# Kernel optimization log

Measured on AMD Instinct MI355X. Metric: run time of the kernel, lower is better.

The kernel has to match this reference:

```python
import jax, jax.numpy as jnp
import numpy as np

HQ, HK, D = 16, 4, 64
WINDOW = 1024  # sliding-window left size; right=0 (causal)
GATE_CH = 12
RMS_EPS = 1e-8


def rms_norm(x):
    return x * jax.lax.rsqrt(jnp.mean(x * x, axis=-1, keepdims=True) + RMS_EPS)


def apply_rope(x, cos, sin):
    # x: [B,T,H,D]; cos/sin: [T,D//2] broadcast to [1,T,1,D//2]
    x1, x2 = jnp.split(x, 2, axis=-1)
    c = cos[None, :, None, :]
    s = sin[None, :, None, :]
    return jnp.concatenate([x1 * c - x2 * s, x1 * s + x2 * c], axis=-1)


def setup_inputs() -> dict:
    key = jax.random.key(0)
    ks = jax.random.split(key, 7)
    B, T, E = 2, 2048, HQ * D
    x = jax.random.normal(ks[0], (B, T, E), jnp.float32)
    value_embeds = jax.random.normal(ks[1], (B, T, HK * D), jnp.float32)
    # rope cache: angles for half the head dim
    inv_freq = 1.0 / (10000.0 ** (jnp.arange(D // 2, dtype=jnp.float32) / (D // 2)))
    ang = jnp.arange(T, dtype=jnp.float32)[:, None] * inv_freq[None, :]
    rope_cos = jnp.cos(ang)
    rope_sin = jnp.sin(ang)
    std = (3.0 ** 0.5) * (E ** -0.5)
    w_qkv = jax.random.uniform(ks[2], ((HQ + 2 * HK) * D, E), jnp.float32, -std, std)
    w_gate = jax.random.normal(ks[3], (HK, GATE_CH), jnp.float32) * 0.02
    w_o = jax.random.normal(ks[4], (E, E), jnp.float32) * 0.02
    return {"x": x, "value_embeds": value_embeds, "rope_cos": rope_cos,
            "rope_sin": rope_sin, "w_qkv": w_qkv, "w_gate": w_gate, "w_o": w_o}


def reference(x, value_embeds, rope_cos, rope_sin, w_qkv, w_gate, w_o):
    B, T, E = x.shape
    groups = HQ // HK
    qkv = jnp.einsum('bte,fe->btf', x, w_qkv).reshape(B, T, HQ + 2 * HK, D)
    q = qkv[:, :, :HQ, :]
    k = qkv[:, :, HQ:HQ + HK, :]
    v = qkv[:, :, HQ + HK:, :]
    # value-embedding gating
    ve = value_embeds.reshape(B, T, HK, D)
    gate = 3.0 * jax.nn.sigmoid(jnp.einsum('btc,hc->bth', x[..., :GATE_CH], w_gate))
    v = v + gate[..., None] * ve
    # rope + qk-norm
    q = rms_norm(apply_rope(q, rope_cos, rope_sin))
    k = rms_norm(apply_rope(k, rope_cos, rope_sin))
    # GQA: repeat kv heads
    k_rep = jnp.repeat(k, groups, axis=2)  # [B,T,HQ,D]
    v_rep = jnp.repeat(v, groups, axis=2)
    scale = 1.0 / jnp.sqrt(jnp.float32(D))
    scores = jnp.einsum('bqhd,bkhd->bhqk', q, k_rep) * scale
    i = jnp.arange(T)[:, None]
    j = jnp.arange(T)[None, :]
    mask = (j <= i) & (j >= i - WINDOW)  # causal + sliding window
    scores = jnp.where(mask[None, None], scores, jnp.float32(-1e30))
    attn = jax.nn.softmax(scores, axis=-1)
    out = jnp.einsum('bhqk,bkhd->bqhd', attn, v_rep).reshape(B, T, E)
    out = jnp.einsum('bte,fe->btf', out, w_o)
    return out
```

## Files before the change

kernel.cpp:

```cpp
#include <hip/hip_runtime.h>
#include <math.h>

#define T_LEN 2048
#define NB 2
#define E_DIM 1024
#define F_DIM 1536
#define HQn 16
#define HKn 4
#define Dh 64
#define WIN 1024
#define GATE_CH 12
#define PS 72

typedef unsigned short u16;
typedef unsigned int u32;
typedef __attribute__((ext_vector_type(8))) short bf16x8;
typedef __attribute__((ext_vector_type(4))) short bf16x4;
typedef __attribute__((ext_vector_type(4))) float f32x4;

#if __has_builtin(__builtin_amdgcn_mfma_f32_16x16x16bf16_1k)
#define MFMA16(A, B, C) __builtin_amdgcn_mfma_f32_16x16x16bf16_1k(A, B, C, 0, 0, 0)
#elif __has_builtin(__builtin_amdgcn_mfma_f32_16x16x16_bf16)
#define MFMA16(A, B, C) __builtin_amdgcn_mfma_f32_16x16x16_bf16(A, B, C, 0, 0, 0)
#else
static __device__ __forceinline__ f32x4 mfma16_asm(bf16x4 a, bf16x4 b, f32x4 c) {
  f32x4 d;
  asm volatile("s_nop 1\n\tv_mfma_f32_16x16x16_bf16 %0, %1, %2, %3\n\ts_nop 7\n\ts_nop 7"
               : "=v"(d) : "v"(a), "v"(b), "v"(c));
  return d;
}
#define MFMA16(A, B, C) mfma16_asm(A, B, C)
#endif

__device__ __forceinline__ u16 f2bf(float f) {
  union { float f; unsigned int u; } v; v.f = f;
  unsigned int u = v.u + 0x7FFF + ((v.u >> 16) & 1);
  return (u16)(u >> 16);
}
__device__ __forceinline__ float bf2f(u16 h) {
  union { unsigned int u; float f; } v; v.u = ((unsigned int)h) << 16;
  return v.f;
}
__device__ __forceinline__ u32 pack_bf2(float hi, float lo) {
  union { float f; u32 u; } a, b; a.f = hi; b.f = lo;
  return __builtin_amdgcn_perm(a.u + 0x8000u, b.u + 0x8000u, 0x07060302u);
}
__device__ __forceinline__ void async_copy16(const void* g, void* l) {
  __builtin_amdgcn_global_load_lds(
      (const __attribute__((address_space(1))) unsigned int*)g,
      (__attribute__((address_space(3))) unsigned int*)l, 16, 0, 0);
}

__global__ __launch_bounds__(256) void cvt_all(
    const float4* __restrict__ x, const float4* __restrict__ wqkv,
    const float4* __restrict__ wo, uint2* __restrict__ xb,
    uint2* __restrict__ wqb, uint2* __restrict__ wob)
{
  int blk = blockIdx.x;
  const float4* in; uint2* out; int i;
  if (blk < 4096)       { in = x;    out = xb;  i = blk * 256 + threadIdx.x; }
  else if (blk < 5632)  { in = wqkv; out = wqb; i = (blk - 4096) * 256 + threadIdx.x; }
  else                  { in = wo;   out = wob; i = (blk - 5632) * 256 + threadIdx.x; }
  float4 v = in[i];
  uint2 o;
  o.x = (unsigned)f2bf(v.x) | ((unsigned)f2bf(v.y) << 16);
  o.y = (unsigned)f2bf(v.z) | ((unsigned)f2bf(v.w) << 16);
  out[i] = o;
}

template<int BM, int BN, int STORE_BF16>
__global__ __launch_bounds__(256) void gemm_bf16(
    const u16* __restrict__ A, const u16* __restrict__ B,
    void* __restrict__ Cv, int M, int N, int K)
{
  constexpr int MI = BM / 32, NJ = BN / 32;
  __shared__ u16 As[BM * 32];
  __shared__ u16 Bs[BN * 32];
  const int tid = threadIdx.x;
  const int wave = tid >> 6, lane = tid & 63;
  const int quad = lane >> 4, lanelow = lane & 15;
  const int row0 = blockIdx.x * BM;
  const int col0 = blockIdx.y * BN;
  const int wm = (wave >> 1) * (BM / 2), wn = (wave & 1) * (BN / 2);

  f32x4 acc[MI][NJ];
#pragma unroll
  for (int i = 0; i < MI; ++i)
#pragma unroll
    for (int j = 0; j < NJ; ++j) acc[i][j] = (f32x4){0.f, 0.f, 0.f, 0.f};

  const int r1 = wave * 16 + (lane >> 2);
  const int c1 = (lane & 3) * 8;

  for (int k0 = 0; k0 < K; k0 += 32) {
    __syncthreads();
#pragma unroll
    for (int p = 0; p < BM / 64; ++p)
      async_copy16(A + (size_t)(row0 + r1 + p * 64) * K + k0 + c1,
                   &As[(r1 + p * 64) * 32 + c1]);
#pragma unroll
    for (int p = 0; p < BN / 64; ++p)
      async_copy16(B + (size_t)(col0 + r1 + p * 64) * K + k0 + c1,
                   &Bs[(r1 + p * 64) * 32 + c1]);
    __syncthreads();

    bf16x8 a[MI], b[NJ];
#pragma unroll
    for (int i = 0; i < MI; ++i)
      a[i] = *(const bf16x8*)&As[(wm + i * 16 + lanelow) * 32 + quad * 8];
#pragma unroll
    for (int j = 0; j < NJ; ++j)
      b[j] = *(const bf16x8*)&Bs[(wn + j * 16 + lanelow) * 32 + quad * 8];
#pragma unroll
    for (int i = 0; i < MI; ++i)
#pragma unroll
      for (int j = 0; j < NJ; ++j)
        acc[i][j] = __builtin_amdgcn_mfma_f32_16x16x32_bf16(a[i], b[j], acc[i][j], 0, 0, 0);
  }

#pragma unroll
  for (int i = 0; i < MI; ++i)
#pragma unroll
    for (int j = 0; j < NJ; ++j) {
      int r = row0 + wm + i * 16 + quad * 4;
      int c = col0 + wn + j * 16 + lanelow;
#pragma unroll
      for (int reg = 0; reg < 4; ++reg) {
        if (STORE_BF16)
          ((u16*)Cv)[(size_t)(r + reg) * N + c] = f2bf(acc[i][j][reg]);
        else
          ((float*)Cv)[(size_t)(r + reg) * N + c] = acc[i][j][reg];
      }
    }
}

__global__ __launch_bounds__(256) void postproc_bf(
    const u16* __restrict__ qkv, const float* __restrict__ x,
    const float* __restrict__ ve, const float* __restrict__ rcos,
    const float* __restrict__ rsin, const float* __restrict__ wg,
    u16* __restrict__ qa, u16* __restrict__ ka, u16* __restrict__ va)
{
  const int token = blockIdx.x;
  const int t = token & (T_LEN - 1);
  const int tid = threadIdx.x;
  const int wave = tid >> 6, lane = tid & 63;
  __shared__ float gate[HKn];
  if (tid < HKn) {
    float g = 0.f;
#pragma unroll
    for (int c = 0; c < GATE_CH; ++c)
      g += x[(size_t)token * E_DIM + c] * wg[tid * GATE_CH + c];
    gate[tid] = 3.f / (1.f + __expf(-g));
  }
  __syncthreads();
  const int half = lane & 31;
  for (int vi = wave; vi < HQn + HKn; vi += 4) {
    const u16* p = qkv + (size_t)token * F_DIM + vi * Dh;
    float c = rcos[t * 32 + half], s = rsin[t * 32 + half];
    float x1 = bf2f(p[half]), x2 = bf2f(p[half + 32]);
    float y = (lane < 32) ? (x1 * c - x2 * s) : (x1 * s + x2 * c);
    float ss = y * y;
#pragma unroll
    for (int o = 32; o; o >>= 1) ss += __shfl_xor(ss, o, 64);
    float v = y * rsqrtf(ss * (1.f / Dh) + 1e-8f);
    if (vi < HQn)
      qa[((size_t)token * HQn + vi) * Dh + lane] = f2bf(v * 0.1803368801f);
    else
      ka[((size_t)token * HKn + (vi - HQn)) * Dh + lane] = f2bf(v);
  }
  {
    float g = gate[tid >> 6];
    size_t vidx = (size_t)token * (HKn * Dh) + tid;
    va[vidx] = f2bf(bf2f(qkv[(size_t)token * F_DIM + (HQn + HKn) * Dh + tid]) + g * ve[vidx]);
  }
}

__global__ __launch_bounds__(256) void transpose_v(
    const u16* __restrict__ va, u16* __restrict__ vt)
{
  __shared__ u16 tile[64][PS];
  const int bhk = blockIdx.y;
  const int b = bhk >> 2, hk = bhk & 3;
  const int t0 = blockIdx.x * 64;
  const int tid = threadIdx.x;
#pragma unroll
  for (int p = 0; p < 2; ++p) {
    int s = tid + p * 256;
    int r = s >> 3, seg = s & 7;
    *(uint4*)&tile[r][seg * 8] =
        *(const uint4*)(va + ((size_t)(b * T_LEN + t0 + r) * HKn + hk) * Dh + seg * 8);
  }
  __syncthreads();
#pragma unroll
  for (int p = 0; p < 2; ++p) {
    int s = tid + p * 256;
    int d = s >> 3, seg = s & 7;
    u16 tmp[8];
#pragma unroll
    for (int e = 0; e < 8; ++e) tmp[e] = tile[seg * 8 + e][d];
    *(uint4*)(vt + ((size_t)bhk * Dh + d) * T_LEN + t0 + seg * 8) = *(uint4*)tmp;
  }
}

__global__ __launch_bounds__(256) void attn_mfma(
    const u16* __restrict__ qa, const u16* __restrict__ ka,
    const u16* __restrict__ vt_g, u16* __restrict__ att)
{
  __shared__ u16 Ks[2][64 * PS];
  __shared__ u16 Vt[2][64 * PS];
  const int qt = blockIdx.x, h = blockIdx.y, b = blockIdx.z;
  const int hk = h >> 2;
  const int qb = qt * 64;
  const int tid = threadIdx.x;
  const int wave = tid >> 6, lane = tid & 63;
  const int quad = lane >> 4, lanelow = lane & 15;

  bf16x8 aQ[2];
#pragma unroll
  for (int kk = 0; kk < 2; ++kk)
    aQ[kk] = *(const bf16x8*)(qa +
        ((size_t)(b * T_LEN + qb + wave * 16 + lanelow) * HQn + h) * Dh +
        kk * 32 + quad * 8);

  f32x4 O[4];
  float l = 0.f;
#pragma unroll
  for (int dt = 0; dt < 4; ++dt) O[dt] = (f32x4){0.f, 0.f, 0.f, 0.f};

  const int kt0 = (qt >= 16) ? qt - 16 : 0;
  const int kt1 = qt;

  const int sr0 = tid >> 3,         sc0 = (tid & 7) * 8;
  const int sr1 = (tid + 256) >> 3, sc1 = ((tid + 256) & 7) * 8;
  const u16* kg = ka + (size_t)(b * T_LEN) * (HKn * Dh) + hk * Dh;
  const u16* vg = vt_g + (size_t)(b * HKn + hk) * Dh * T_LEN;

  {
    const int kb = kt0 * 64;
    uint4 k0 = *(const uint4*)(kg + (size_t)(kb + sr0) * (HKn * Dh) + sc0);
    uint4 k1 = *(const uint4*)(kg + (size_t)(kb + sr1) * (HKn * Dh) + sc1);
    uint4 v0 = *(const uint4*)(vg + (size_t)sr0 * T_LEN + kb + sc0);
    uint4 v1 = *(const uint4*)(vg + (size_t)sr1 * T_LEN + kb + sc1);
    *(uint4*)&Ks[0][sr0 * PS + sc0] = k0;
    *(uint4*)&Ks[0][sr1 * PS + sc1] = k1;
    *(uint4*)&Vt[0][sr0 * PS + sc0] = v0;
    *(uint4*)&Vt[0][sr1 * PS + sc1] = v1;
  }

  for (int kt = kt0; kt <= kt1; ++kt) {
    const int buf = (kt - kt0) & 1;
    const int kb = kt * 64;
    uint4 k0, k1, v0, v1;
    const bool more = (kt < kt1);
    if (more) {
      const int nb = kb + 64;
      k0 = *(const uint4*)(kg + (size_t)(nb + sr0) * (HKn * Dh) + sc0);
      k1 = *(const uint4*)(kg + (size_t)(nb + sr1) * (HKn * Dh) + sc1);
      v0 = *(const uint4*)(vg + (size_t)sr0 * T_LEN + nb + sc0);
      v1 = *(const uint4*)(vg + (size_t)sr1 * T_LEN + nb + sc1);
    }
    __syncthreads();

    f32x4 St[4];
#pragma unroll
    for (int jt = 0; jt < 4; ++jt) {
      bf16x8 aK0 = *(const bf16x8*)&Ks[buf][(jt * 16 + lanelow) * PS + quad * 8];
      bf16x8 aK1 = *(const bf16x8*)&Ks[buf][(jt * 16 + lanelow) * PS + 32 + quad * 8];
      f32x4 acc = (f32x4){-12.f, -12.f, -12.f, -12.f};
      acc = __builtin_amdgcn_mfma_f32_16x16x32_bf16(aK0, aQ[0], acc, 0, 0, 0);
      acc = __builtin_amdgcn_mfma_f32_16x16x32_bf16(aK1, aQ[1], acc, 0, 0, 0);
      St[jt] = acc;
    }
    if (kt == kt1) {
#pragma unroll
      for (int jt = 0; jt < 4; ++jt)
#pragma unroll
        for (int rr = 0; rr < 4; ++rr) {
          int ig = qb + wave * 16 + lanelow;
          int jg = kb + jt * 16 + quad * 4 + rr;
          if (jg > ig) St[jt][rr] = -1e30f;
        }
    } else if (kt == kt0 && qt >= 16) {
#pragma unroll
      for (int jt = 0; jt < 4; ++jt)
#pragma unroll
        for (int rr = 0; rr < 4; ++rr) {
          int ig = qb + wave * 16 + lanelow;
          int jg = kb + jt * 16 + quad * 4 + rr;
          if (jg < ig - WIN) St[jt][rr] = -1e30f;
        }
    }
    bf16x4 Pt[4];
#pragma unroll
    for (int jt = 0; jt < 4; ++jt) {
      float p0 = __builtin_amdgcn_exp2f(St[jt][0]);
      float p1 = __builtin_amdgcn_exp2f(St[jt][1]);
      float p2 = __builtin_amdgcn_exp2f(St[jt][2]);
      float p3 = __builtin_amdgcn_exp2f(St[jt][3]);
      l += (p0 + p1) + (p2 + p3);
      union { uint2 u; bf16x4 v; } pu;
      pu.u.x = pack_bf2(p1, p0);
      pu.u.y = pack_bf2(p3, p2);
      Pt[jt] = pu.v;
    }
#pragma unroll
    for (int dt = 0; dt < 4; ++dt)
#pragma unroll
      for (int jt = 0; jt < 4; ++jt) {
        bf16x4 aV = *(const bf16x4*)&Vt[buf][(dt * 16 + lanelow) * PS + jt * 16 + quad * 4];
        O[dt] = MFMA16(aV, Pt[jt], O[dt]);
      }
    if (more) {
      const int nbuf = buf ^ 1;
      *(uint4*)&Ks[nbuf][sr0 * PS + sc0] = k0;
      *(uint4*)&Ks[nbuf][sr1 * PS + sc1] = k1;
      *(uint4*)&Vt[nbuf][sr0 * PS + sc0] = v0;
      *(uint4*)&Vt[nbuf][sr1 * PS + sc1] = v1;
    }
  }

  {
    float s = l;
    s += __shfl_xor(s, 16, 64);
    s += __shfl_xor(s, 32, 64);
    float inv = 1.f / s;
    int qg = qb + wave * 16 + lanelow;
    u16* obase = att + (size_t)(b * T_LEN + qg) * E_DIM + h * Dh;
#pragma unroll
    for (int dt = 0; dt < 4; ++dt) {
      bf16x4 ov;
      ov[0] = (short)f2bf(O[dt][0] * inv);
      ov[1] = (short)f2bf(O[dt][1] * inv);
      ov[2] = (short)f2bf(O[dt][2] * inv);
      ov[3] = (short)f2bf(O[dt][3] * inv);
      *(bf16x4*)(obase + dt * 16 + quad * 4) = ov;
    }
  }
}

extern "C" void kernel_launch(void* const* d_in, const int* in_sizes, int n_in,
                              void* d_out, int out_size, void* d_ws, size_t ws_size,
                              hipStream_t stream)
{
  const float* x    = (const float*)d_in[0];
  const float* ve   = (const float*)d_in[1];
  const float* rc   = (const float*)d_in[2];
  const float* rs   = (const float*)d_in[3];
  const float* wqkv = (const float*)d_in[4];
  const float* wg   = (const float*)d_in[5];
  const float* wo   = (const float*)d_in[6];
  float* out = (float*)d_out;

  char* ws = (char*)d_ws;
  u16* x_bf    = (u16*)(ws);
  u16* v_t     = x_bf;
  u16* wqkv_bf = (u16*)(ws + 8388608);
  u16* wo_bf   = (u16*)(ws + 11534336);
  u16* qkv_bf  = (u16*)(ws + 13631488);
  u16* att     = qkv_bf;
  u16* q_att   = (u16*)(ws + 26214400);
  u16* k_att   = (u16*)(ws + 34603008);
  u16* v_att   = (u16*)(ws + 36700160);

  cvt_all<<<6656, 256, 0, stream>>>((const float4*)x, (const float4*)wqkv,
                                    (const float4*)wo, (uint2*)x_bf,
                                    (uint2*)wqkv_bf, (uint2*)wo_bf);
  gemm_bf16<128, 64, 1><<<dim3(32, 24), 256, 0, stream>>>(x_bf, wqkv_bf, qkv_bf, 4096, F_DIM, E_DIM);
  postproc_bf<<<NB * T_LEN, 256, 0, stream>>>(qkv_bf, x, ve, rc, rs, wg, q_att, k_att, v_att);
  transpose_v<<<dim3(32, 8), 256, 0, stream>>>(v_att, v_t);
  attn_mfma<<<dim3(T_LEN / 64, HQn, NB), 256, 0, stream>>>(q_att, k_att, v_t, att);
  gemm_bf16<64, 64, 0><<<dim3(64, 16), 256, 0, stream>>>(att, wo_bf, out, 4096, E_DIM, E_DIM);
}
```

Before: 181.6 us.

## Fuse x bf16 conversion into QKV GEMM and double-buffer GEMM LDS tiles

Removes the separate fp32-to-bf16 conversion of x. The QKV GEMM now loads fp32 A tiles and packs them to bf16 in registers before writing to LDS. Both GEMMs switch from single-buffered async global-to-LDS copies to register-staged double buffering, so the next tile's global load overlaps the current tile's MFMAs with one barrier per step. This saves a full pass over x (write and re-read) but doubles LDS use, adds register pressure, and reads twice the bytes for A in the QKV GEMM.

Result: no change. 184.9 us (+1.9%).

```diff
diff --git a/kernel.cpp b/kernel.cpp
--- a/kernel.cpp
+++ b/kernel.cpp
@@ -45,22 +45,15 @@
   union { float f; u32 u; } a, b; a.f = hi; b.f = lo;
   return __builtin_amdgcn_perm(a.u + 0x8000u, b.u + 0x8000u, 0x07060302u);
 }
-__device__ __forceinline__ void async_copy16(const void* g, void* l) {
-  __builtin_amdgcn_global_load_lds(
-      (const __attribute__((address_space(1))) unsigned int*)g,
-      (__attribute__((address_space(3))) unsigned int*)l, 16, 0, 0);
-}
-
-__global__ __launch_bounds__(256) void cvt_all(
-    const float4* __restrict__ x, const float4* __restrict__ wqkv,
-    const float4* __restrict__ wo, uint2* __restrict__ xb,
+
+__global__ __launch_bounds__(256) void cvt_w(
+    const float4* __restrict__ wqkv, const float4* __restrict__ wo,
     uint2* __restrict__ wqb, uint2* __restrict__ wob)
 {
   int blk = blockIdx.x;
   const float4* in; uint2* out; int i;
-  if (blk < 4096)       { in = x;    out = xb;  i = blk * 256 + threadIdx.x; }
-  else if (blk < 5632)  { in = wqkv; out = wqb; i = (blk - 4096) * 256 + threadIdx.x; }
-  else                  { in = wo;   out = wob; i = (blk - 5632) * 256 + threadIdx.x; }
+  if (blk < 1536) { in = wqkv; out = wqb; i = blk * 256 + threadIdx.x; }
+  else            { in = wo;   out = wob; i = (blk - 1536) * 256 + threadIdx.x; }
   float4 v = in[i];
   uint2 o;
   o.x = (unsigned)f2bf(v.x) | ((unsigned)f2bf(v.y) << 16);
@@ -68,14 +61,16 @@
   out[i] = o;
 }
 
-template<int BM, int BN, int STORE_BF16>
-__global__ __launch_bounds__(256) void gemm_bf16(
-    const u16* __restrict__ A, const u16* __restrict__ B,
+template<int BM, int BN, int AF32, int STORE_BF16>
+__global__ __launch_bounds__(256) void gemm_dbuf(
+    const void* __restrict__ Av, const u16* __restrict__ B,
     void* __restrict__ Cv, int M, int N, int K)
 {
   constexpr int MI = BM / 32, NJ = BN / 32;
-  __shared__ u16 As[BM * 32];
-  __shared__ u16 Bs[BN * 32];
+  constexpr int NSA = BM * 4 / 256;
+  constexpr int NSB = BN * 4 / 256;
+  __shared__ u16 As[2][BM * 32];
+  __shared__ u16 Bs[2][BN * 32];
   const int tid = threadIdx.x;
   const int wave = tid >> 6, lane = tid & 63;
   const int quad = lane >> 4, lanelow = lane & 15;
@@ -83,39 +78,88 @@
   const int col0 = blockIdx.y * BN;
   const int wm = (wave >> 1) * (BM / 2), wn = (wave & 1) * (BN / 2);
 
+  const float* Af = (const float*)Av;
+  const u16*  Ah = (const u16*)Av;
+
   f32x4 acc[MI][NJ];
 #pragma unroll
   for (int i = 0; i < MI; ++i)
 #pragma unroll
     for (int j = 0; j < NJ; ++j) acc[i][j] = (f32x4){0.f, 0.f, 0.f, 0.f};
 
-  const int r1 = wave * 16 + (lane >> 2);
-  const int c1 = (lane & 3) * 8;
+  int arow[NSA], acol[NSA];
+#pragma unroll
+  for (int s = 0; s < NSA; ++s) {
+    int slot = tid + s * 256;
+    arow[s] = slot >> 2; acol[s] = (slot & 3) * 8;
+  }
+  int brow[NSB], bcol[NSB];
+#pragma unroll
+  for (int s = 0; s < NSB; ++s) {
+    int slot = tid + s * 256;
+    brow[s] = slot >> 2; bcol[s] = (slot & 3) * 8;
+  }
+
+  uint4 aU[NSA]; float4 aF0[NSA], aF1[NSA];
+  uint4 bU[NSB];
+
+  auto loadT = [&](int k0) {
+#pragma unroll
+    for (int s = 0; s < NSA; ++s) {
+      if (AF32) {
+        const float* p = Af + (size_t)(row0 + arow[s]) * K + k0 + acol[s];
+        aF0[s] = *(const float4*)p;
+        aF1[s] = *(const float4*)(p + 4);
+      } else {
+        aU[s] = *(const uint4*)(Ah + (size_t)(row0 + arow[s]) * K + k0 + acol[s]);
+      }
+    }
+#pragma unroll
+    for (int s = 0; s < NSB; ++s)
+      bU[s] = *(const uint4*)(B + (size_t)(col0 + brow[s]) * K + k0 + bcol[s]);
+  };
+  auto storeT = [&](int buf) {
+#pragma unroll
+    for (int s = 0; s < NSA; ++s) {
+      uint4 w;
+      if (AF32) {
+        w.x = pack_bf2(aF0[s].y, aF0[s].x);
+        w.y = pack_bf2(aF0[s].w, aF0[s].z);
+        w.z = pack_bf2(aF1[s].y, aF1[s].x);
+        w.w = pack_bf2(aF1[s].w, aF1[s].z);
+      } else {
+        w = aU[s];
+      }
+      *(uint4*)&As[buf][arow[s] * 32 + acol[s]] = w;
+    }
+#pragma unroll
+    for (int s = 0; s < NSB; ++s)
+      *(uint4*)&Bs[buf][brow[s] * 32 + bcol[s]] = bU[s];
+  };
+
+  loadT(0);
+  storeT(0);
 
   for (int k0 = 0; k0 < K; k0 += 32) {
+    const int buf = (k0 >> 5) & 1;
+    const bool more = (k0 + 32) < K;
+    if (more) loadT(k0 + 32);
     __syncthreads();
-#pragma unroll
-    for (int p = 0; p < BM / 64; ++p)
-      async_copy16(A + (size_t)(row0 + r1 + p * 64) * K + k0 + c1,
-                   &As[(r1 + p * 64) * 32 + c1]);
-#pragma unroll
-    for (int p = 0; p < BN / 64; ++p)
-      async_copy16(B + (size_t)(col0 + r1 + p * 64) * K + k0 + c1,
-                   &Bs[(r1 + p * 64) * 32 + c1]);
-    __syncthreads();
 
     bf16x8 a[MI], b[NJ];
 #pragma unroll
     for (int i = 0; i < MI; ++i)
-      a[i] = *(const bf16x8*)&As[(wm + i * 16 + lanelow) * 32 + quad * 8];
+      a[i] = *(const bf16x8*)&As[buf][(wm + i * 16 + lanelow) * 32 + quad * 8];
 #pragma unroll
     for (int j = 0; j < NJ; ++j)
-      b[j] = *(const bf16x8*)&Bs[(wn + j * 16 + lanelow) * 32 + quad * 8];
+      b[j] = *(const bf16x8*)&Bs[buf][(wn + j * 16 + lanelow) * 32 + quad * 8];
 #pragma unroll
     for (int i = 0; i < MI; ++i)
 #pragma unroll
       for (int j = 0; j < NJ; ++j)
         acc[i][j] = __builtin_amdgcn_mfma_f32_16x16x32_bf16(a[i], b[j], acc[i][j], 0, 0, 0);
+
+    if (more) storeT(buf ^ 1);
   }
 
 #pragma unroll
@@ -352,22 +396,22 @@
   float* out = (float*)d_out;
 
   char* ws = (char*)d_ws;
-  u16* x_bf    = (u16*)(ws);
-  u16* v_t     = x_bf;
-  u16* wqkv_bf = (u16*)(ws + 8388608);
-  u16* wo_bf   = (u16*)(ws + 11534336);
-  u16* qkv_bf  = (u16*)(ws + 13631488);
+  u16* v_t     = (u16*)(ws);
+  u16* wqkv_bf = (u16*)(ws + 2097152);
+  u16* wo_bf   = (u16*)(ws + 5242880);
+  u16* qkv_bf  = (u16*)(ws + 7340032);
   u16* att     = qkv_bf;
-  u16* q_att   = (u16*)(ws + 26214400);
-  u16* k_att   = (u16*)(ws + 34603008);
-  u16* v_att   = (u16*)(ws + 36700160);
-
-  cvt_all<<<6656, 256, 0, stream>>>((const float4*)x, (const float4*)wqkv,
-                                    (const float4*)wo, (uint2*)x_bf,
-                                    (uint2*)wqkv_bf, (uint2*)wo_bf);
-  gemm_bf16<128, 64, 1><<<dim3(32, 24), 256, 0, stream>>>(x_bf, wqkv_bf, qkv_bf, 4096, F_DIM, E_DIM);
+  u16* q_att   = (u16*)(ws + 19922944);
+  u16* k_att   = (u16*)(ws + 28311552);
+  u16* v_att   = (u16*)(ws + 30408704);
+
+  cvt_w<<<2560, 256, 0, stream>>>((const float4*)wqkv, (const float4*)wo,
+                                  (uint2*)wqkv_bf, (uint2*)wo_bf);
+  gemm_dbuf<128, 64, 1, 1><<<dim3(32, 24), 256, 0, stream>>>(
+      x, wqkv_bf, qkv_bf, 4096, F_DIM, E_DIM);
   postproc_bf<<<NB * T_LEN, 256, 0, stream>>>(qkv_bf, x, ve, rc, rs, wg, q_att, k_att, v_att);
   transpose_v<<<dim3(32, 8), 256, 0, stream>>>(v_att, v_t);
   attn_mfma<<<dim3(T_LEN / 64, HQn, NB), 256, 0, stream>>>(q_att, k_att, v_t, att);
-  gemm_bf16<64, 64, 0><<<dim3(64, 16), 256, 0, stream>>>(att, wo_bf, out, 4096, E_DIM, E_DIM);
-}
+  gemm_dbuf<64, 64, 0, 0><<<dim3(64, 16), 256, 0, stream>>>(
+      att, wo_bf, out, 4096, E_DIM, E_DIM);
+}
```
